# Kernel optimization log

Hardware: AMD Instinct MI355X
Metric: run time of the kernel (lower is better)

The kernel has to match this reference:

```python
import jax, jax.numpy as jnp
import numpy as np

B, N, F, E = 2, 50000, 128, 500000


def setup_inputs() -> dict:
    key = jax.random.key(0)
    ks = jax.random.split(key, 7)
    x0 = jax.random.normal(ks[0], (B, N, F), dtype=jnp.float32)
    dst = jax.random.randint(ks[1], (E,), 0, N, dtype=jnp.int32)
    src = jax.random.randint(ks[2], (E,), 0, N, dtype=jnp.int32)
    # torch Linear weights: [out_features, in_features]
    w0 = jax.random.normal(ks[3], (F, 2 * F), dtype=jnp.float32) * 0.05
    b0 = jax.random.normal(ks[4], (F,), dtype=jnp.float32) * 0.05
    w1 = jax.random.normal(ks[5], (F, F), dtype=jnp.float32) * 0.05
    b1 = jax.random.normal(ks[6], (F,), dtype=jnp.float32) * 0.05
    return {"x0": x0, "dst": dst, "src": src, "w0": w0, "b0": b0, "w1": w1, "b1": b1}


def reference(x0, dst, src, w0, b0, w1, b1):
    n = x0.shape[1]
    # gather source node features per edge: [B, E, F] -> [E, B, F] for segment ops
    xe = jnp.transpose(x0[:, src], (1, 0, 2))
    # scatter-reduce over destination nodes (include_self=False semantics)
    s = jax.ops.segment_sum(xe, dst, num_segments=n)                      # [N, B, F]
    mx = jax.ops.segment_max(xe, dst, num_segments=n)                     # [N, B, F]
    cnt = jax.ops.segment_sum(jnp.ones((dst.shape[0],), x0.dtype), dst, num_segments=n)  # [N]
    has_edge = (cnt > 0)[:, None, None]
    x0t = jnp.transpose(x0, (1, 0, 2))                                    # [N, B, F]
    # nodes with no incoming edges keep their original values
    mean = jnp.where(has_edge, s / jnp.maximum(cnt, 1.0)[:, None, None], x0t)
    amax = jnp.where(has_edge, mx, x0t)
    x = jnp.concatenate([mean, amax], axis=-1)                            # [N, B, 2F]
    h = jax.nn.relu(jnp.einsum('nbf,of->nbo', x, w0) + b0)
    # dropout is identity in eval mode
    out = x0t + jnp.einsum('nbf,of->nbo', h, w1) + b1
    return jnp.transpose(out, (1, 0, 2))                                  # [B, N, F]
```

## Files before the change

### kernel.cpp

```cpp
#include <hip/hip_runtime.h>

#define NN 50000
#define FF 128
constexpr int NBF2 = NN * 256;
constexpr int CAP  = 64;
constexpr int CSTR = 16;

typedef __attribute__((ext_vector_type(4))) short short4v;
typedef __attribute__((ext_vector_type(8))) short short8;
typedef __attribute__((ext_vector_type(4))) float floatx4;

__device__ __forceinline__ unsigned short f2bf(float x) {
    unsigned int u = __float_as_uint(x);
    unsigned int r = (u + 0x7fff + ((u >> 16) & 1)) >> 16;
    return (unsigned short)r;
}
__device__ __forceinline__ float bf2f(short x) {
    return __uint_as_float(((unsigned int)(unsigned short)x) << 16);
}

__global__ __launch_bounds__(256)
void convert_fill(const int* __restrict__ dst, const int* __restrict__ src, int E,
                  const float* __restrict__ x0,
                  const float* __restrict__ w0, const float* __restrict__ w1,
                  int* __restrict__ cursor, unsigned short* __restrict__ esrc,
                  unsigned short* __restrict__ x0b,
                  unsigned short* __restrict__ w0b, unsigned short* __restrict__ w1b) {
    int i = blockIdx.x * 256 + threadIdx.x;
    if (i < E) {
        int d = dst[i];
        int pos = atomicAdd(&cursor[d * CSTR], 1);
        if (pos < CAP) esrc[d * CAP + pos] = (unsigned short)src[i];
    }
    int stride = gridDim.x * 256;
    for (int p = i; p < NBF2 / 4; p += stride) {
        int v0 = p * 4;
        int n = v0 >> 8;
        int b = (v0 >> 7) & 1;
        int f = v0 & 127;
        const float4 in = *(const float4*)&x0[(b * NN + n) * FF + f];
        short4v o = { (short)f2bf(in.x), (short)f2bf(in.y), (short)f2bf(in.z), (short)f2bf(in.w) };
        *(short4v*)&x0b[v0] = o;
    }
    if (i < 128 * 256) w0b[i] = f2bf(w0[i]);
    if (i < 128 * 128) w1b[i] = f2bf(w1[i]);
}

constexpr int NPB = 8;
constexpr int XCP = 256 + 8;
constexpr int HSP = 128 + 8;

__global__ __launch_bounds__(256, 8)
void fused_gcn(const unsigned short* __restrict__ x0b,
               const float* __restrict__ x0,
               const int* __restrict__ deg,
               const unsigned short* __restrict__ esrc,
               const unsigned short* __restrict__ w0b,
               const float* __restrict__ b0,
               const unsigned short* __restrict__ w1b,
               const float* __restrict__ b1,
               float* __restrict__ out) {
    __shared__ unsigned short xc[16 * XCP];
    __shared__ unsigned short hs[16 * HSP];

    int t = threadIdx.x;
    int q = t >> 6;
    int l = t & 63;
    int n0 = blockIdx.x * NPB;
    int nA = n0 + q * 2;
    int nB = nA + 1;

    int l4 = l * 4;
    int bb = l >> 5;
    int ff = (l & 31) * 4;
    const float NEG_INF = __int_as_float(0xFF800000);

    int vA = esrc[nA * CAP + l];
    int vB = esrc[nB * CAP + l];
    int dA = min(__builtin_amdgcn_readfirstlane(deg[nA * CSTR]), CAP);
    int dB = min(__builtin_amdgcn_readfirstlane(deg[nB * CSTR]), CAP);

    float sA0=0,sA1=0,sA2=0,sA3=0, sB0=0,sB1=0,sB2=0,sB3=0;
    float mA0=NEG_INF,mA1=NEG_INF,mA2=NEG_INF,mA3=NEG_INF;
    float mB0=NEG_INF,mB1=NEG_INF,mB2=NEG_INF,mB3=NEG_INF;

#define ACCV(r, S0,S1,S2,S3, M0,M1,M2,M3) { \
    float v0=bf2f(r[0]), v1=bf2f(r[1]), v2=bf2f(r[2]), v3=bf2f(r[3]); \
    S0+=v0; S1+=v1; S2+=v2; S3+=v3; \
    M0=fmaxf(M0,v0); M1=fmaxf(M1,v1); M2=fmaxf(M2,v2); M3=fmaxf(M3,v3); }

#define GLOOP(vv, dd, S0,S1,S2,S3, M0,M1,M2,M3) \
    for (int k = 0; k < dd; k += 8) { \
        int u0 = __builtin_amdgcn_readlane(vv, k + 0); u0 = (u0 < NN) ? u0 : 0; \
        int u1 = __builtin_amdgcn_readlane(vv, k + 1); u1 = (u1 < NN) ? u1 : 0; \
        int u2 = __builtin_amdgcn_readlane(vv, k + 2); u2 = (u2 < NN) ? u2 : 0; \
        int u3 = __builtin_amdgcn_readlane(vv, k + 3); u3 = (u3 < NN) ? u3 : 0; \
        int u4 = __builtin_amdgcn_readlane(vv, k + 4); u4 = (u4 < NN) ? u4 : 0; \
        int u5 = __builtin_amdgcn_readlane(vv, k + 5); u5 = (u5 < NN) ? u5 : 0; \
        int u6 = __builtin_amdgcn_readlane(vv, k + 6); u6 = (u6 < NN) ? u6 : 0; \
        int u7 = __builtin_amdgcn_readlane(vv, k + 7); u7 = (u7 < NN) ? u7 : 0; \
        short4v r0 = *(const short4v*)&x0b[(u0 << 8) + l4]; \
        short4v r1 = *(const short4v*)&x0b[(u1 << 8) + l4]; \
        short4v r2 = *(const short4v*)&x0b[(u2 << 8) + l4]; \
        short4v r3 = *(const short4v*)&x0b[(u3 << 8) + l4]; \
        short4v r4 = *(const short4v*)&x0b[(u4 << 8) + l4]; \
        short4v r5 = *(const short4v*)&x0b[(u5 << 8) + l4]; \
        short4v r6 = *(const short4v*)&x0b[(u6 << 8) + l4]; \
        short4v r7 = *(const short4v*)&x0b[(u7 << 8) + l4]; \
        ACCV(r0, S0,S1,S2,S3, M0,M1,M2,M3) \
        if (k + 1 < dd) ACCV(r1, S0,S1,S2,S3, M0,M1,M2,M3) \
        if (k + 2 < dd) ACCV(r2, S0,S1,S2,S3, M0,M1,M2,M3) \
        if (k + 3 < dd) ACCV(r3, S0,S1,S2,S3, M0,M1,M2,M3) \
        if (k + 4 < dd) ACCV(r4, S0,S1,S2,S3, M0,M1,M2,M3) \
        if (k + 5 < dd) ACCV(r5, S0,S1,S2,S3, M0,M1,M2,M3) \
        if (k + 6 < dd) ACCV(r6, S0,S1,S2,S3, M0,M1,M2,M3) \
        if (k + 7 < dd) ACCV(r7, S0,S1,S2,S3, M0,M1,M2,M3) \
    }

    GLOOP(vA, dA, sA0,sA1,sA2,sA3, mA0,mA1,mA2,mA3)
    GLOOP(vB, dB, sB0,sB1,sB2,sB3, mB0,mB1,mB2,mB3)
#undef GLOOP
#undef ACCV

#define FINAL_N(g, nn, dgx, S0,S1,S2,S3, M0,M1,M2,M3) { \
    float me0,me1,me2,me3,a0,a1,a2,a3; \
    if (dgx > 0) { \
        float inv = 1.0f / (float)dgx; \
        me0=S0*inv; me1=S1*inv; me2=S2*inv; me3=S3*inv; \
        a0=M0; a1=M1; a2=M2; a3=M3; \
    } else { \
        short4v rr = *(const short4v*)&x0b[((nn) << 8) + l4]; \
        me0=a0=bf2f(rr[0]); me1=a1=bf2f(rr[1]); me2=a2=bf2f(rr[2]); me3=a3=bf2f(rr[3]); \
    } \
    int row = (q * 2 + g) * 2 + bb; \
    short4v mv = { (short)f2bf(me0),(short)f2bf(me1),(short)f2bf(me2),(short)f2bf(me3) }; \
    short4v av = { (short)f2bf(a0),(short)f2bf(a1),(short)f2bf(a2),(short)f2bf(a3) }; \
    *(short4v*)&xc[row * XCP + ff]       = mv; \
    *(short4v*)&xc[row * XCP + 128 + ff] = av; \
}
    FINAL_N(0, nA, dA, sA0,sA1,sA2,sA3, mA0,mA1,mA2,mA3)
    FINAL_N(1, nB, dB, sB0,sB1,sB2,sB3, mB0,mB1,mB2,mB3)
#undef FINAL_N
    __syncthreads();

    int m    = l & 15;
    int quad = l >> 4;
    int colbase = q * 32;

    floatx4 acc[2];
#pragma unroll
    for (int ct = 0; ct < 2; ++ct) acc[ct] = (floatx4){0.f, 0.f, 0.f, 0.f};
#pragma unroll
    for (int ks = 0; ks < 8; ++ks) {
        short8 a = *(const short8*)&xc[m * XCP + ks * 32 + quad * 8];
#pragma unroll
        for (int ct = 0; ct < 2; ++ct) {
            short8 bfr = *(const short8*)&w0b[(colbase + ct * 16 + m) * 256 + ks * 32 + quad * 8];
            acc[ct] = __builtin_amdgcn_mfma_f32_16x16x32_bf16(a, bfr, acc[ct], 0, 0, 0);
        }
    }
#pragma unroll
    for (int ct = 0; ct < 2; ++ct) {
        int col = colbase + ct * 16 + m;
        float bias = b0[col];
#pragma unroll
        for (int r = 0; r < 4; ++r) {
            int row = quad * 4 + r;
            hs[row * HSP + col] = f2bf(fmaxf(acc[ct][r] + bias, 0.0f));
        }
    }
    __syncthreads();

    floatx4 acc2[2];
#pragma unroll
    for (int ct = 0; ct < 2; ++ct) acc2[ct] = (floatx4){0.f, 0.f, 0.f, 0.f};
#pragma unroll
    for (int ks = 0; ks < 4; ++ks) {
        short8 a = *(const short8*)&hs[m * HSP + ks * 32 + quad * 8];
#pragma unroll
        for (int ct = 0; ct < 2; ++ct) {
            short8 bfr = *(const short8*)&w1b[(colbase + ct * 16 + m) * 128 + ks * 32 + quad * 8];
            acc2[ct] = __builtin_amdgcn_mfma_f32_16x16x32_bf16(a, bfr, acc2[ct], 0, 0, 0);
        }
    }
#pragma unroll
    for (int ct = 0; ct < 2; ++ct) {
        int col = colbase + ct * 16 + m;
        float bias = b1[col];
#pragma unroll
        for (int r = 0; r < 4; ++r) {
            int row = quad * 4 + r;
            int n  = n0 + (row >> 1);
            int b2 = row & 1;
            int oi = (b2 * NN + n) * FF + col;
            out[oi] = x0[oi] + bias + acc2[ct][r];
        }
    }
}

extern "C" void kernel_launch(void* const* d_in, const int* in_sizes, int n_in,
                              void* d_out, int out_size, void* d_ws, size_t ws_size,
                              hipStream_t stream) {
    const float* x0  = (const float*)d_in[0];
    const int*   dst = (const int*)d_in[1];
    const int*   src = (const int*)d_in[2];
    const float* w0  = (const float*)d_in[3];
    const float* b0  = (const float*)d_in[4];
    const float* w1  = (const float*)d_in[5];
    const float* b1  = (const float*)d_in[6];
    float* out = (float*)d_out;
    int E = in_sizes[1];

    int* cursor = (int*)d_ws;
    unsigned short* esrc = (unsigned short*)(cursor + (size_t)NN * CSTR);
    unsigned short* x0b  = esrc + (size_t)NN * CAP;
    unsigned short* w0b  = x0b + NBF2;
    unsigned short* w1b  = w0b + 128 * 256;

    int eb = (E + 255) / 256;

    hipMemsetAsync(cursor, 0, (size_t)NN * CSTR * sizeof(int), stream);
    convert_fill<<<eb, 256, 0, stream>>>(dst, src, E, x0, w0, w1, cursor, esrc, x0b, w0b, w1b);
    fused_gcn<<<NN / NPB, 256, 0, stream>>>(x0b, x0, cursor, esrc, w0b, b0, w1b, b1, out);
}
```

Baseline: 243.2 us.

## Gather two neighbors per wave with 16-byte loads and add nontemporal streaming

The neighbor gather is restructured so each half-wave loads a different neighbor's full 256-element bf16 row using 8-wide (16-byte) loads instead of 4-wide loads. The two halves are then combined with cross-lane shuffles for sum and max. This halves the number of load instructions and loop iterations per neighbor and gives wider memory transactions. The cost is the shuffle reduction, extra accumulator registers and tail handling for odd degrees. Nontemporal loads and stores are also applied to the streamed x0 reads and the output writes so they do not pollute the cache.

```diff
diff --git a/kernel.cpp b/kernel.cpp
--- a/kernel.cpp
+++ b/kernel.cpp
@@ -38,7 +38,7 @@
         int n = v0 >> 8;
         int b = (v0 >> 7) & 1;
         int f = v0 & 127;
-        const float4 in = *(const float4*)&x0[(b * NN + n) * FF + f];
+        floatx4 in = __builtin_nontemporal_load((const floatx4*)&x0[(b * NN + n) * FF + f]);
         short4v o = { (short)f2bf(in.x), (short)f2bf(in.y), (short)f2bf(in.z), (short)f2bf(in.w) };
         *(short4v*)&x0b[v0] = o;
     }
@@ -70,9 +70,8 @@
     int nA = n0 + q * 2;
     int nB = nA + 1;
 
-    int l4 = l * 4;
-    int bb = l >> 5;
-    int ff = (l & 31) * 4;
+    bool hi = (l >= 32);
+    int fo8 = (l & 31) * 8;
     const float NEG_INF = __int_as_float(0xFF800000);
 
     int vA = esrc[nA * CAP + l];
@@ -80,67 +79,81 @@
     int dA = min(__builtin_amdgcn_readfirstlane(deg[nA * CSTR]), CAP);
     int dB = min(__builtin_amdgcn_readfirstlane(deg[nB * CSTR]), CAP);
 
-    float sA0=0,sA1=0,sA2=0,sA3=0, sB0=0,sB1=0,sB2=0,sB3=0;
-    float mA0=NEG_INF,mA1=NEG_INF,mA2=NEG_INF,mA3=NEG_INF;
-    float mB0=NEG_INF,mB1=NEG_INF,mB2=NEG_INF,mB3=NEG_INF;
-
-#define ACCV(r, S0,S1,S2,S3, M0,M1,M2,M3) { \
+#define ACC8(r) { \
     float v0=bf2f(r[0]), v1=bf2f(r[1]), v2=bf2f(r[2]), v3=bf2f(r[3]); \
-    S0+=v0; S1+=v1; S2+=v2; S3+=v3; \
-    M0=fmaxf(M0,v0); M1=fmaxf(M1,v1); M2=fmaxf(M2,v2); M3=fmaxf(M3,v3); }
-
-#define GLOOP(vv, dd, S0,S1,S2,S3, M0,M1,M2,M3) \
-    for (int k = 0; k < dd; k += 8) { \
-        int u0 = __builtin_amdgcn_readlane(vv, k + 0); u0 = (u0 < NN) ? u0 : 0; \
-        int u1 = __builtin_amdgcn_readlane(vv, k + 1); u1 = (u1 < NN) ? u1 : 0; \
-        int u2 = __builtin_amdgcn_readlane(vv, k + 2); u2 = (u2 < NN) ? u2 : 0; \
-        int u3 = __builtin_amdgcn_readlane(vv, k + 3); u3 = (u3 < NN) ? u3 : 0; \
-        int u4 = __builtin_amdgcn_readlane(vv, k + 4); u4 = (u4 < NN) ? u4 : 0; \
-        int u5 = __builtin_amdgcn_readlane(vv, k + 5); u5 = (u5 < NN) ? u5 : 0; \
-        int u6 = __builtin_amdgcn_readlane(vv, k + 6); u6 = (u6 < NN) ? u6 : 0; \
-        int u7 = __builtin_amdgcn_readlane(vv, k + 7); u7 = (u7 < NN) ? u7 : 0; \
-        short4v r0 = *(const short4v*)&x0b[(u0 << 8) + l4]; \
-        short4v r1 = *(const short4v*)&x0b[(u1 << 8) + l4]; \
-        short4v r2 = *(const short4v*)&x0b[(u2 << 8) + l4]; \
-        short4v r3 = *(const short4v*)&x0b[(u3 << 8) + l4]; \
-        short4v r4 = *(const short4v*)&x0b[(u4 << 8) + l4]; \
-        short4v r5 = *(const short4v*)&x0b[(u5 << 8) + l4]; \
-        short4v r6 = *(const short4v*)&x0b[(u6 << 8) + l4]; \
-        short4v r7 = *(const short4v*)&x0b[(u7 << 8) + l4]; \
-        ACCV(r0, S0,S1,S2,S3, M0,M1,M2,M3) \
-        if (k + 1 < dd) ACCV(r1, S0,S1,S2,S3, M0,M1,M2,M3) \
-        if (k + 2 < dd) ACCV(r2, S0,S1,S2,S3, M0,M1,M2,M3) \
-        if (k + 3 < dd) ACCV(r3, S0,S1,S2,S3, M0,M1,M2,M3) \
-        if (k + 4 < dd) ACCV(r4, S0,S1,S2,S3, M0,M1,M2,M3) \
-        if (k + 5 < dd) ACCV(r5, S0,S1,S2,S3, M0,M1,M2,M3) \
-        if (k + 6 < dd) ACCV(r6, S0,S1,S2,S3, M0,M1,M2,M3) \
-        if (k + 7 < dd) ACCV(r7, S0,S1,S2,S3, M0,M1,M2,M3) \
-    }
-
-    GLOOP(vA, dA, sA0,sA1,sA2,sA3, mA0,mA1,mA2,mA3)
-    GLOOP(vB, dB, sB0,sB1,sB2,sB3, mB0,mB1,mB2,mB3)
-#undef GLOOP
-#undef ACCV
-
-#define FINAL_N(g, nn, dgx, S0,S1,S2,S3, M0,M1,M2,M3) { \
-    float me0,me1,me2,me3,a0,a1,a2,a3; \
-    if (dgx > 0) { \
-        float inv = 1.0f / (float)dgx; \
-        me0=S0*inv; me1=S1*inv; me2=S2*inv; me3=S3*inv; \
-        a0=M0; a1=M1; a2=M2; a3=M3; \
-    } else { \
-        short4v rr = *(const short4v*)&x0b[((nn) << 8) + l4]; \
-        me0=a0=bf2f(rr[0]); me1=a1=bf2f(rr[1]); me2=a2=bf2f(rr[2]); me3=a3=bf2f(rr[3]); \
-    } \
-    int row = (q * 2 + g) * 2 + bb; \
-    short4v mv = { (short)f2bf(me0),(short)f2bf(me1),(short)f2bf(me2),(short)f2bf(me3) }; \
-    short4v av = { (short)f2bf(a0),(short)f2bf(a1),(short)f2bf(a2),(short)f2bf(a3) }; \
-    *(short4v*)&xc[row * XCP + ff]       = mv; \
-    *(short4v*)&xc[row * XCP + 128 + ff] = av; \
-}
-    FINAL_N(0, nA, dA, sA0,sA1,sA2,sA3, mA0,mA1,mA2,mA3)
-    FINAL_N(1, nB, dB, sB0,sB1,sB2,sB3, mB0,mB1,mB2,mB3)
-#undef FINAL_N
+    float v4=bf2f(r[4]), v5=bf2f(r[5]), v6=bf2f(r[6]), v7=bf2f(r[7]); \
+    S0+=v0;S1+=v1;S2+=v2;S3+=v3;S4+=v4;S5+=v5;S6+=v6;S7+=v7; \
+    M0=fmaxf(M0,v0);M1=fmaxf(M1,v1);M2=fmaxf(M2,v2);M3=fmaxf(M3,v3); \
+    M4=fmaxf(M4,v4);M5=fmaxf(M5,v5);M6=fmaxf(M6,v6);M7=fmaxf(M7,v7); }
+
+#define PAIR_LOAD(vv, k, rname) \
+    int ue##rname = __builtin_amdgcn_readlane(vv, (k));     ue##rname = (ue##rname < NN) ? ue##rname : 0; \
+    int uo##rname = __builtin_amdgcn_readlane(vv, (k) + 1); uo##rname = (uo##rname < NN) ? uo##rname : 0; \
+    int us##rname = hi ? uo##rname : ue##rname; \
+    short8 rname = *(const short8*)&x0b[(us##rname << 8) + fo8];
+
+#define GATHER_NODE(vv, dd, nn, g) { \
+    float S0=0,S1=0,S2=0,S3=0,S4=0,S5=0,S6=0,S7=0; \
+    float M0=NEG_INF,M1=NEG_INF,M2=NEG_INF,M3=NEG_INF; \
+    float M4=NEG_INF,M5=NEG_INF,M6=NEG_INF,M7=NEG_INF; \
+    int kk = 0; \
+    for (; kk + 7 < dd; kk += 8) {           \
+        PAIR_LOAD(vv, kk,     ra) PAIR_LOAD(vv, kk + 2, rb) \
+        PAIR_LOAD(vv, kk + 4, rc) PAIR_LOAD(vv, kk + 6, rd) \
+        ACC8(ra) ACC8(rb) ACC8(rc) ACC8(rd) \
+    } \
+    if (kk + 3 < dd) { \
+        PAIR_LOAD(vv, kk, ra) PAIR_LOAD(vv, kk + 2, rb) \
+        ACC8(ra) ACC8(rb) \
+        kk += 4; \
+    } \
+    if (kk + 1 < dd) { \
+        PAIR_LOAD(vv, kk, ra) \
+        ACC8(ra) \
+        kk += 2; \
+    } \
+    if (dd & 1) {                             \
+        int ut = __builtin_amdgcn_readlane(vv, dd - 1); ut = (ut < NN) ? ut : 0; \
+        short8 rt = *(const short8*)&x0b[(ut << 8) + fo8]; \
+        if (!hi) { ACC8(rt) } \
+    } \
+     \
+    { float o; \
+      o=__shfl_xor(S0,32); S0+=o; o=__shfl_xor(S1,32); S1+=o; \
+      o=__shfl_xor(S2,32); S2+=o; o=__shfl_xor(S3,32); S3+=o; \
+      o=__shfl_xor(S4,32); S4+=o; o=__shfl_xor(S5,32); S5+=o; \
+      o=__shfl_xor(S6,32); S6+=o; o=__shfl_xor(S7,32); S7+=o; \
+      o=__shfl_xor(M0,32); M0=fmaxf(M0,o); o=__shfl_xor(M1,32); M1=fmaxf(M1,o); \
+      o=__shfl_xor(M2,32); M2=fmaxf(M2,o); o=__shfl_xor(M3,32); M3=fmaxf(M3,o); \
+      o=__shfl_xor(M4,32); M4=fmaxf(M4,o); o=__shfl_xor(M5,32); M5=fmaxf(M5,o); \
+      o=__shfl_xor(M6,32); M6=fmaxf(M6,o); o=__shfl_xor(M7,32); M7=fmaxf(M7,o); } \
+    if (!hi) { \
+        float e0,e1,e2,e3,e4,e5,e6,e7, a0,a1,a2,a3,a4,a5,a6,a7; \
+        if (dd > 0) { \
+            float inv = 1.0f / (float)dd; \
+            e0=S0*inv;e1=S1*inv;e2=S2*inv;e3=S3*inv;e4=S4*inv;e5=S5*inv;e6=S6*inv;e7=S7*inv; \
+            a0=M0;a1=M1;a2=M2;a3=M3;a4=M4;a5=M5;a6=M6;a7=M7; \
+        } else { \
+            short8 rr = *(const short8*)&x0b[((nn) << 8) + fo8]; \
+            e0=a0=bf2f(rr[0]); e1=a1=bf2f(rr[1]); e2=a2=bf2f(rr[2]); e3=a3=bf2f(rr[3]); \
+            e4=a4=bf2f(rr[4]); e5=a5=bf2f(rr[5]); e6=a6=bf2f(rr[6]); e7=a7=bf2f(rr[7]); \
+        } \
+        int row = (q * 2 + g) * 2 + (l >> 4);       \
+        int fb  = (l & 15) * 8; \
+        short8 mv = { (short)f2bf(e0),(short)f2bf(e1),(short)f2bf(e2),(short)f2bf(e3), \
+                      (short)f2bf(e4),(short)f2bf(e5),(short)f2bf(e6),(short)f2bf(e7) }; \
+        short8 av = { (short)f2bf(a0),(short)f2bf(a1),(short)f2bf(a2),(short)f2bf(a3), \
+                      (short)f2bf(a4),(short)f2bf(a5),(short)f2bf(a6),(short)f2bf(a7) }; \
+        *(short8*)&xc[row * XCP + fb]       = mv; \
+        *(short8*)&xc[row * XCP + 128 + fb] = av; \
+    } \
+}
+
+    GATHER_NODE(vA, dA, nA, 0)
+    GATHER_NODE(vB, dB, nB, 1)
+#undef GATHER_NODE
+#undef PAIR_LOAD
+#undef ACC8
     __syncthreads();
 
     int m    = l & 15;
@@ -193,7 +206,8 @@
             int n  = n0 + (row >> 1);
             int b2 = row & 1;
             int oi = (b2 * NN + n) * FF + col;
-            out[oi] = x0[oi] + bias + acc2[ct][r];
+            float xv = __builtin_nontemporal_load(&x0[oi]);
+            __builtin_nontemporal_store(xv + bias + acc2[ct][r], &out[oi]);
         }
     }
 }
```

Result: faster. 236.4 us (-2.8%).
